# Kernel optimization log

Hardware: AMD Instinct MI355X
Metric: run time of the kernel (lower is better)

## Reference

```python
import jax, jax.numpy as jnp
import numpy as np

DIM = 768
HEADS = 12
HD = DIM // HEADS
E = 8
R = 64
ALPHA = 128.0
LORA_SCALE = ALPHA / R  # 2.0
ENABLE_BITS = np.array([1.0, 0.0, 1.0], dtype=np.float32)  # LoRA on q and v slices of qkv


def setup_inputs() -> dict:
    key = jax.random.key(0)
    ks = jax.random.split(key, 8)
    x = jax.random.normal(ks[0], (2, 4096, DIM), jnp.float32)
    # base (frozen) weights, shared across experts; no biases (qkv_bias=False)
    Wqkv = jax.random.normal(ks[1], (3 * DIM, DIM), jnp.float32) * 0.02
    Wproj = jax.random.normal(ks[2], (DIM, DIM), jnp.float32) * 0.02
    # per-expert LoRA adapters. qkv: shared down-proj A, per-output-slice up-proj B,
    # masked by enable bits (q,k,v).
    Aqkv = jax.random.normal(ks[3], (E, R, DIM), jnp.float32) * 0.02
    Bqkv = jax.random.normal(ks[4], (E, 3, DIM, R), jnp.float32) * 0.02
    Bqkv = Bqkv * jnp.asarray(ENABLE_BITS)[None, :, None, None]
    Aproj = jax.random.normal(ks[5], (E, R, DIM), jnp.float32) * 0.02
    Bproj = jax.random.normal(ks[6], (E, DIM, R), jnp.float32) * 0.02
    expert_indices = np.arange(4, dtype=np.int64) % E  # static per-chunk routing
    chunk_sizes = np.array([1024, 1024, 1024, 1024], dtype=np.int64)
    return {"x": x, "Wqkv": Wqkv, "Aqkv": Aqkv, "Bqkv": Bqkv, "Wproj": Wproj,
            "Aproj": Aproj, "Bproj": Bproj, "expert_indices": expert_indices,
            "chunk_sizes": chunk_sizes}


def reference(x, Wqkv, Aqkv, Bqkv, Wproj, Aproj, Bproj, expert_indices, chunk_sizes):
    # chunk sizes / expert indices are static host-side routing metadata
    sizes = [int(c) for c in np.asarray(chunk_sizes)]
    eidx = [int(e) for e in np.asarray(expert_indices)]
    offs = np.concatenate([[0], np.cumsum(sizes)])
    B = x.shape[0]
    scale = HD ** -0.5
    last_k = None
    last_v = None
    outs = []
    for i, n in enumerate(sizes):
        xc = x[:, offs[i]:offs[i + 1]]            # [B, n, DIM]
        e = eidx[i]
        # LoRA-adapted qkv for this chunk's expert
        base = xc @ Wqkv.T                        # [B, n, 3*DIM]
        h = xc @ Aqkv[e].T                        # [B, n, R]
        delta = jnp.einsum('bnr,tdr->bntd', h, Bqkv[e]).reshape(B, n, 3 * DIM)
        qkv = (base + LORA_SCALE * delta).reshape(B, n, 3, HEADS, HD)
        qkv = qkv.transpose(2, 0, 3, 1, 4)        # [3, B, H, n, HD]
        q, k, v = qkv[0], qkv[1], qkv[2]
        if last_k is not None:                    # growing KV over chunks (chunk-causal)
            k = jnp.concatenate([last_k, k], axis=-2)
            v = jnp.concatenate([last_v, v], axis=-2)
        last_k, last_v = k, v
        attn = jax.nn.softmax(jnp.einsum('bhqd,bhkd->bhqk', q * scale, k), axis=-1)
        o = jnp.einsum('bhqk,bhkd->bhqd', attn, v)
        o = o.transpose(0, 2, 1, 3).reshape(B, n, DIM)
        # LoRA-adapted output projection for the same expert
        o = o @ Wproj.T + LORA_SCALE * ((o @ Aproj[e].T) @ Bproj[e].T)
        outs.append(o)
    return jnp.concatenate(outs, axis=1)          # [B, total, DIM]
```

## Files before the change

### kernel.cpp

```cpp
#include <hip/hip_runtime.h>
#include <math.h>

#define BATCH   2
#define SEQ     4096
#define DIMD    768
#define NHEADS  12
#define HDIM    64
#define RR      64
#define CHUNK   1024
#define NTOK    (BATCH * SEQ)
#define BHN     (BATCH * NHEADS)
#define KC2     2304
#define QSCALE  0.18033688011112042f

typedef __attribute__((ext_vector_type(8))) short short8;
typedef __attribute__((ext_vector_type(4))) float f32x4;

#define AS1 __attribute__((address_space(1)))
#define AS3 __attribute__((address_space(3)))

__device__ __forceinline__ void glds16(const void* g, void* l) {
    __builtin_amdgcn_global_load_lds((const AS1 unsigned int*)g,
                                     (AS3 unsigned int*)l, 16, 0, 0);
}

__device__ __forceinline__ unsigned short f2bf(float x) {
    union { float f; unsigned u; } c; c.f = x;
    unsigned u = c.u + 0x7fffu + ((c.u >> 16) & 1u);
    return (unsigned short)(u >> 16);
}
__device__ __forceinline__ float bf2f(unsigned short h) {
    union { unsigned u; float f; } c; c.u = ((unsigned)h) << 16;
    return c.f;
}
__device__ __forceinline__ unsigned pack2bf(float a, float b) {
    union { float f; unsigned u; } x, y; x.f = a; y.f = b;
    unsigned ua = x.u + 0x7fffu + ((x.u >> 16) & 1u);
    unsigned ub = y.u + 0x7fffu + ((y.u >> 16) & 1u);
    return (ua >> 16) | (ub & 0xffff0000u);
}

__global__ __launch_bounds__(256)
void combine_split(const float* __restrict__ W, const float* __restrict__ A,
                   const float* __restrict__ Bm, int NB,
                   unsigned short* __restrict__ out)
{
    const int tid = threadIdx.x;
    const int ty = tid >> 4, tx = tid & 15;
    const int f0 = blockIdx.x * 64, d0 = blockIdx.y * 64, e = blockIdx.z;

    __shared__ float Bb[64][68];
    __shared__ float Aa[64][68];

    const float* Ae = A + (long)e * RR * DIMD;
    const float* Be = Bm + (long)e * NB * RR;

    const int lrow = tid >> 2, lc = (tid & 3) * 16;
    #pragma unroll
    for (int u = 0; u < 16; u += 4) {
        *(float4*)&Bb[lrow][lc + u] = *(const float4*)&Be[(long)(f0 + lrow) * RR + lc + u];
        *(float4*)&Aa[lrow][lc + u] = *(const float4*)&Ae[(long)lrow * DIMD + d0 + lc + u];
    }
    __syncthreads();

    float acc[4][4] = {};
    #pragma unroll 4
    for (int r = 0; r < RR; r++) {
        const float4 bv = *(float4*)&Aa[r][tx * 4];
        #pragma unroll
        for (int i = 0; i < 4; i++) {
            const float av = Bb[ty + 16 * i][r];
            acc[i][0] = fmaf(av, bv.x, acc[i][0]);
            acc[i][1] = fmaf(av, bv.y, acc[i][1]);
            acc[i][2] = fmaf(av, bv.z, acc[i][2]);
            acc[i][3] = fmaf(av, bv.w, acc[i][3]);
        }
    }

    #pragma unroll
    for (int i = 0; i < 4; i++) {
        const int f = f0 + ty + 16 * i;
        const int d = d0 + tx * 4;
        unsigned short* o = out + ((long)e * NB + f) * KC2 + d;
        const float4 wv = *(const float4*)&W[(long)f * DIMD + d];
        const float v0 = wv.x + 2.0f * acc[i][0];
        const float v1 = wv.y + 2.0f * acc[i][1];
        const float v2 = wv.z + 2.0f * acc[i][2];
        const float v3 = wv.w + 2.0f * acc[i][3];
        const unsigned short h0 = f2bf(v0), h1 = f2bf(v1);
        const unsigned short h2 = f2bf(v2), h3 = f2bf(v3);
        uint2 hp, lp;
        hp.x = (unsigned)h0 | ((unsigned)h1 << 16);
        hp.y = (unsigned)h2 | ((unsigned)h3 << 16);
        lp.x = pack2bf(v0 - bf2f(h0), v1 - bf2f(h1));
        lp.y = pack2bf(v2 - bf2f(h2), v3 - bf2f(h3));
        *(uint2*)&o[0]    = hp;
        *(uint2*)&o[768]  = lp;
        *(uint2*)&o[1536] = hp;
    }
}

__global__ __launch_bounds__(192)
void build_xa2(const float* __restrict__ X, unsigned short* __restrict__ out)
{
    const int tok = blockIdx.x;
    const int j = threadIdx.x * 4;
    const float* xr = X + (long)tok * DIMD;
    unsigned short* o = out + (long)tok * KC2;
    float4 v = *(const float4*)&xr[j];
    unsigned short h0 = f2bf(v.x), h1 = f2bf(v.y), h2 = f2bf(v.z), h3 = f2bf(v.w);
    uint2 hp, lp;
    hp.x = (unsigned)h0 | ((unsigned)h1 << 16);
    hp.y = (unsigned)h2 | ((unsigned)h3 << 16);
    lp.x = pack2bf(v.x - bf2f(h0), v.y - bf2f(h1));
    lp.y = pack2bf(v.z - bf2f(h2), v.w - bf2f(h3));
    *(uint2*)&o[j] = hp;
    *(uint2*)&o[768 + j] = hp;
    *(uint2*)&o[1536 + j] = lp;
}

template<int MODE>
__global__ __launch_bounds__(256)
void mfma_gemm(const unsigned short* __restrict__ A,
               const unsigned short* __restrict__ B, int NB, int n_base,
               unsigned short* __restrict__ qpl, unsigned short* __restrict__ kpl,
               unsigned short* __restrict__ vpl, float* __restrict__ outf)
{
    __shared__ __align__(16) unsigned short lA[128 * 64];
    __shared__ __align__(16) unsigned short lB[128 * 64];

    const int tid = threadIdx.x;
    const int lane = tid & 63;
    const int wave = tid >> 6;
    const int n = lane & 15;
    const int quad = lane >> 4;
    const int wm = wave & 1, wn = wave >> 1;

    const int m0 = blockIdx.x * 128;
    const int n0 = n_base + blockIdx.y * 128;
    const int e = (m0 & (SEQ - 1)) >> 10;
    const unsigned short* Ap = A + (long)m0 * KC2;
    const unsigned short* Bp = B + ((long)e * NB + n0) * KC2;

    long soff[4];
    int sldsoff = wave * 1024;
    #pragma unroll
    for (int iss = 0; iss < 4; iss++) {
        const int g = iss * 256 + tid;
        const int row = g >> 3;
        const int gc = (g & 7) ^ (row & 7);
        soff[iss] = (long)row * KC2 + gc * 8;
    }

    f32x4 acc[4][4];
    #pragma unroll
    for (int i = 0; i < 4; i++)
        #pragma unroll
        for (int j = 0; j < 4; j++)
            acc[i][j] = (f32x4){0.f, 0.f, 0.f, 0.f};

    for (int k0 = 0; k0 < KC2; k0 += 64) {
        __syncthreads();
        #pragma unroll
        for (int iss = 0; iss < 4; iss++) {
            glds16(Ap + soff[iss] + k0, (char*)lA + iss * 4096 + sldsoff);
            glds16(Bp + soff[iss] + k0, (char*)lB + iss * 4096 + sldsoff);
        }
        __builtin_amdgcn_s_waitcnt(0);
        __syncthreads();

        #pragma unroll
        for (int kk = 0; kk < 2; kk++) {
            const int kg = kk * 4;
            short8 af[4], bfr[4];
            #pragma unroll
            for (int mt = 0; mt < 4; mt++) {
                const int r = wm * 64 + mt * 16 + n;
                const int p = (kg + quad) ^ (r & 7);
                af[mt] = *(const short8*)&lA[r * 64 + p * 8];
            }
            #pragma unroll
            for (int nt = 0; nt < 4; nt++) {
                const int r = wn * 64 + nt * 16 + n;
                const int p = (kg + quad) ^ (r & 7);
                bfr[nt] = *(const short8*)&lB[r * 64 + p * 8];
            }
            #pragma unroll
            for (int mt = 0; mt < 4; mt++)
                #pragma unroll
                for (int nt = 0; nt < 4; nt++) {
                    if (MODE == 1)
                        acc[mt][nt] = __builtin_amdgcn_mfma_f32_16x16x32_bf16(
                            af[mt], bfr[nt], acc[mt][nt], 0, 0, 0);
                    else
                        acc[mt][nt] = __builtin_amdgcn_mfma_f32_16x16x32_bf16(
                            bfr[nt], af[mt], acc[mt][nt], 0, 0, 0);
                }
        }
    }

    #pragma unroll
    for (int mt = 0; mt < 4; mt++) {
        #pragma unroll
        for (int nt = 0; nt < 4; nt++) {
            f32x4 a = acc[mt][nt];
            if (MODE == 0) {
                const int fb = n0 + wn * 64 + nt * 16 + quad * 4;
                const int t = fb >= 768 ? 1 : 0;
                const int rem = fb - t * 768;
                const int head = rem >> 6;
                const int d0 = rem & 63;
                const int token = m0 + wm * 64 + mt * 16 + n;
                const int b = token >> 12, s = token & (SEQ - 1);
                const int bh = b * NHEADS + head;
                const float sc = t ? 1.0f : QSCALE;
                unsigned short* dst = (t ? kpl : qpl) + ((long)(bh * SEQ + s)) * HDIM + d0;
                uint2 pk;
                pk.x = pack2bf(a[0] * sc, a[1] * sc);
                pk.y = pack2bf(a[2] * sc, a[3] * sc);
                *(uint2*)dst = pk;
            } else if (MODE == 1) {
                const int f = n0 + wn * 64 + nt * 16 + n;
                const int head = (f - 1536) >> 6;
                const int d = f & 63;
                const int tok0 = m0 + wm * 64 + mt * 16 + quad * 4;
                const int b = tok0 >> 12, s0 = tok0 & (SEQ - 1);
                const int bh = b * NHEADS + head;
                unsigned short* dst = vpl + ((long)(bh * HDIM + d)) * SEQ + s0;
                uint2 pk;
                pk.x = pack2bf(a[0], a[1]);
                pk.y = pack2bf(a[2], a[3]);
                *(uint2*)dst = pk;
            } else {
                const int fb = n0 + wn * 64 + nt * 16 + quad * 4;
                const int token = m0 + wm * 64 + mt * 16 + n;
                *(f32x4*)&outf[(long)token * DIMD + fb] = a;
            }
        }
    }
}

__global__ __launch_bounds__(256)
void attn_split(const unsigned short* __restrict__ qp,
                const unsigned short* __restrict__ kpl,
                const unsigned short* __restrict__ vtp,
                unsigned short* __restrict__ XA,
                float* __restrict__ pO, float* __restrict__ pl)
{
    __shared__ __align__(16) unsigned short lK[64 * 64];
    __shared__ __align__(16) unsigned short lV[64 * 64];
    __shared__ __align__(16) unsigned short lP[4][32 * 64];

    const int tid = threadIdx.x;
    const int lane = tid & 63;
    const int wave = tid >> 6;
    const int n = lane & 15;
    const int quad = lane >> 4;
    const int c7 = n & 7;

    const int qb = blockIdx.x;
    const int bh = blockIdx.y;
    const int z = blockIdx.z;
    int ci, ks0, klen, pidx;
    switch (z) {
        case 0:  ci = 3; ks0 = 0;    klen = 2048; pidx = 0;  break;
        case 1:  ci = 3; ks0 = 2048; klen = 2048; pidx = 1;  break;
        case 2:  ci = 2; ks0 = 0;    klen = 2048; pidx = 2;  break;
        case 3:  ci = 1; ks0 = 0;    klen = 2048; pidx = -1; break;
        case 4:  ci = 2; ks0 = 2048; klen = 1024; pidx = 3;  break;
        default: ci = 0; ks0 = 0;    klen = 1024; pidx = -1; break;
    }
    const int b = bh / NHEADS;
    const int h = bh - b * NHEADS;

    const long planeQK = (long)bh * SEQ * HDIM;
    const long planeVt = (long)bh * HDIM * SEQ;
    const int qch = qb * 128 + wave * 32;
    const int q0 = ci * CHUNK + qch;

    long skoff[2], svoff[2];
    #pragma unroll
    for (int p = 0; p < 2; p++) {
        const int g = (wave * 2 + p) * 64 + lane;
        const int row = g >> 3;
        const int gc = (g & 7) ^ (row & 7);
        skoff[p] = (long)row * HDIM + gc * 8;
        svoff[p] = (long)row * SEQ + gc * 8;
    }

    short8 qf[2][2];
    #pragma unroll
    for (int qt = 0; qt < 2; qt++)
        #pragma unroll
        for (int s = 0; s < 2; s++)
            qf[qt][s] = *(const short8*)&qp[planeQK + (long)(q0 + qt * 16 + n) * HDIM + s * 32 + quad * 8];

    const short8 ones8 = {0x3f80, 0x3f80, 0x3f80, 0x3f80, 0x3f80, 0x3f80, 0x3f80, 0x3f80};

    f32x4 acc[4][2];
    f32x4 accl[2];
    #pragma unroll
    for (int m2 = 0; m2 < 4; m2++) {
        acc[m2][0] = (f32x4){0.f, 0.f, 0.f, 0.f};
        acc[m2][1] = (f32x4){0.f, 0.f, 0.f, 0.f};
    }
    accl[0] = (f32x4){0.f, 0.f, 0.f, 0.f};
    accl[1] = (f32x4){0.f, 0.f, 0.f, 0.f};

    unsigned short* Pw = &lP[wave][0];

    for (int k0 = ks0; k0 < ks0 + klen; k0 += 64) {
        __syncthreads();
        glds16(kpl + planeQK + (long)k0 * HDIM + skoff[0], (char*)lK + wave * 2048);
        glds16(kpl + planeQK + (long)k0 * HDIM + skoff[1], (char*)lK + wave * 2048 + 1024);
        glds16(vtp + planeVt + k0 + svoff[0], (char*)lV + wave * 2048);
        glds16(vtp + planeVt + k0 + svoff[1], (char*)lV + wave * 2048 + 1024);
        __builtin_amdgcn_s_waitcnt(0);
        __syncthreads();

        f32x4 st[4][2];
        #pragma unroll
        for (int kt = 0; kt < 4; kt++) {
            st[kt][0] = (f32x4){0.f, 0.f, 0.f, 0.f};
            st[kt][1] = (f32x4){0.f, 0.f, 0.f, 0.f};
        }
        #pragma unroll
        for (int s = 0; s < 2; s++) {
            #pragma unroll
            for (int kt = 0; kt < 4; kt++) {
                const int gr = (s * 4 + quad) ^ c7;
                short8 kf = *(const short8*)&lK[(kt * 16 + n) * 64 + gr * 8];
                st[kt][0] = __builtin_amdgcn_mfma_f32_16x16x32_bf16(kf, qf[0][s], st[kt][0], 0, 0, 0);
                st[kt][1] = __builtin_amdgcn_mfma_f32_16x16x32_bf16(kf, qf[1][s], st[kt][1], 0, 0, 0);
            }
        }

        #pragma unroll
        for (int qt = 0; qt < 2; qt++) {
            unsigned short* prow = Pw + (qt * 16 + n) * 64;
            #pragma unroll
            for (int kt = 0; kt < 4; kt++) {
                const unsigned u0 = __float_as_uint(__builtin_exp2f(st[kt][qt][0])) + 0x8000u;
                const unsigned u1 = __float_as_uint(__builtin_exp2f(st[kt][qt][1])) + 0x8000u;
                const unsigned u2 = __float_as_uint(__builtin_exp2f(st[kt][qt][2])) + 0x8000u;
                const unsigned u3 = __float_as_uint(__builtin_exp2f(st[kt][qt][3])) + 0x8000u;
                uint2 pkv;
                pkv.x = __builtin_amdgcn_perm(u1, u0, 0x07060302);
                pkv.y = __builtin_amdgcn_perm(u3, u2, 0x07060302);
                const int gsw = (2 * kt + (quad >> 1)) ^ c7;
                *(uint2*)&prow[gsw * 8 + (quad & 1) * 4] = pkv;
            }
        }

        #pragma unroll
        for (int hh = 0; hh < 2; hh++) {
            short8 pf[2];
            #pragma unroll
            for (int qt = 0; qt < 2; qt++) {
                const int gsw = (hh * 4 + quad) ^ c7;
                pf[qt] = *(const short8*)&Pw[(qt * 16 + n) * 64 + gsw * 8];
            }
            #pragma unroll
            for (int m2 = 0; m2 < 4; m2++) {
                const int gr = (hh * 4 + quad) ^ c7;
                short8 vf = *(const short8*)&lV[(m2 * 16 + n) * 64 + gr * 8];
                acc[m2][0] = __builtin_amdgcn_mfma_f32_16x16x32_bf16(vf, pf[0], acc[m2][0], 0, 0, 0);
                acc[m2][1] = __builtin_amdgcn_mfma_f32_16x16x32_bf16(vf, pf[1], acc[m2][1], 0, 0, 0);
            }
            accl[0] = __builtin_amdgcn_mfma_f32_16x16x32_bf16(ones8, pf[0], accl[0], 0, 0, 0);
            accl[1] = __builtin_amdgcn_mfma_f32_16x16x32_bf16(ones8, pf[1], accl[1], 0, 0, 0);
        }
    }

    if (pidx < 0) {
        #pragma unroll
        for (int qt = 0; qt < 2; qt++) {
            const float inv = 1.0f / accl[qt][0];
            const int token = b * SEQ + q0 + qt * 16 + n;
            unsigned short* xrow = XA + (long)token * KC2;
            #pragma unroll
            for (int m2 = 0; m2 < 4; m2++) {
                const int d = h * HDIM + m2 * 16 + quad * 4;
                const float o0 = acc[m2][qt][0] * inv;
                const float o1 = acc[m2][qt][1] * inv;
                const float o2 = acc[m2][qt][2] * inv;
                const float o3 = acc[m2][qt][3] * inv;
                const unsigned short h0 = f2bf(o0), h1 = f2bf(o1);
                const unsigned short h2 = f2bf(o2), h3 = f2bf(o3);
                uint2 hp, lp;
                hp.x = (unsigned)h0 | ((unsigned)h1 << 16);
                hp.y = (unsigned)h2 | ((unsigned)h3 << 16);
                lp.x = pack2bf(o0 - bf2f(h0), o1 - bf2f(h1));
                lp.y = pack2bf(o2 - bf2f(h2), o3 - bf2f(h3));
                *(uint2*)&xrow[d] = hp;
                *(uint2*)&xrow[768 + d] = hp;
                *(uint2*)&xrow[1536 + d] = lp;
            }
        }
    } else {
        const long pq = (long)(pidx * BHN + bh) * 1024 + qch;
        #pragma unroll
        for (int qt = 0; qt < 2; qt++) {
            const long qoff = (pq + qt * 16 + n) * 64;
            #pragma unroll
            for (int m2 = 0; m2 < 4; m2++)
                *(f32x4*)&pO[qoff + m2 * 16 + quad * 4] = acc[m2][qt];
            if (quad == 0)
                pl[pq + qt * 16 + n] = accl[qt][0];
        }
    }
}

__global__ __launch_bounds__(256)
void attn_combine(const float* __restrict__ pO, const float* __restrict__ pl,
                  unsigned short* __restrict__ XA)
{
    const int t = threadIdx.x;
    const int g = blockIdx.x;
    const int ci = 2 + (g >> 3);
    const int qb = g & 7;
    const int bh = blockIdx.y;
    const int b = bh / NHEADS, h = bh - b * NHEADS;
    const int pA = (ci == 2) ? 2 : 0;
    const int pB = (ci == 2) ? 3 : 1;

    const int qrow = t >> 1;
    const int dh = (t & 1) * 32;
    const int qc = qb * 128 + qrow;
    const long iA = (long)(pA * BHN + bh) * 1024 + qc;
    const long iB = (long)(pB * BHN + bh) * 1024 + qc;
    const float inv = 1.0f / (pl[iA] + pl[iB]);
    const int token = b * SEQ + ci * CHUNK + qc;
    unsigned short* xrow = XA + (long)token * KC2 + h * HDIM + dh;

    #pragma unroll
    for (int u = 0; u < 8; u++) {
        const float4 a = *(const float4*)&pO[iA * 64 + dh + u * 4];
        const float4 c = *(const float4*)&pO[iB * 64 + dh + u * 4];
        const float o0 = (a.x + c.x) * inv;
        const float o1 = (a.y + c.y) * inv;
        const float o2 = (a.z + c.z) * inv;
        const float o3 = (a.w + c.w) * inv;
        const unsigned short h0 = f2bf(o0), h1 = f2bf(o1);
        const unsigned short h2 = f2bf(o2), h3 = f2bf(o3);
        uint2 hp, lp;
        hp.x = (unsigned)h0 | ((unsigned)h1 << 16);
        hp.y = (unsigned)h2 | ((unsigned)h3 << 16);
        lp.x = pack2bf(o0 - bf2f(h0), o1 - bf2f(h1));
        lp.y = pack2bf(o2 - bf2f(h2), o3 - bf2f(h3));
        *(uint2*)&xrow[u * 4] = hp;
        *(uint2*)&xrow[768 + u * 4] = hp;
        *(uint2*)&xrow[1536 + u * 4] = lp;
    }
}

extern "C" void kernel_launch(void* const* d_in, const int* in_sizes, int n_in,
                              void* d_out, int out_size, void* d_ws, size_t ws_size,
                              hipStream_t stream) {
    (void)in_sizes; (void)n_in; (void)out_size; (void)ws_size;
    const float* x     = (const float*)d_in[0];
    const float* Wqkv  = (const float*)d_in[1];
    const float* Aqkv  = (const float*)d_in[2];
    const float* Bqkv  = (const float*)d_in[3];
    const float* Wproj = (const float*)d_in[4];
    const float* Aproj = (const float*)d_in[5];
    const float* Bproj = (const float*)d_in[6];

    char* wsb = (char*)d_ws;
    unsigned short* XA   = (unsigned short*)(wsb);
    unsigned short* WBq  = (unsigned short*)(wsb + (38l << 20));
    float*          pO   = (float*)(wsb + (38l << 20));
    float*          pl   = (float*)(wsb + (63l << 20));
    unsigned short* WBp  = (unsigned short*)(wsb + (80l << 20));
    unsigned short* qpl  = (unsigned short*)(wsb + (94l << 20));
    unsigned short* kpl  = (unsigned short*)(wsb + (107l << 20));
    unsigned short* vpl  = (unsigned short*)(wsb + (120l << 20));

    dim3 blk(256);

    combine_split<<<dim3(36, 12, 4), blk, 0, stream>>>(Wqkv, Aqkv, Bqkv, 3 * DIMD, WBq);
    combine_split<<<dim3(12, 12, 4), blk, 0, stream>>>(Wproj, Aproj, Bproj, DIMD, WBp);
    build_xa2<<<dim3(NTOK), dim3(192), 0, stream>>>(x, XA);
    mfma_gemm<0><<<dim3(NTOK / 128, 12), blk, 0, stream>>>(XA, WBq, 3 * DIMD, 0,    qpl, kpl, vpl, nullptr);
    mfma_gemm<1><<<dim3(NTOK / 128, 6),  blk, 0, stream>>>(XA, WBq, 3 * DIMD, 1536, qpl, kpl, vpl, nullptr);
    attn_split<<<dim3(8, BHN, 6), blk, 0, stream>>>(qpl, kpl, vpl, XA, pO, pl);
    attn_combine<<<dim3(16, BHN), blk, 0, stream>>>(pO, pl, XA);
    mfma_gemm<2><<<dim3(NTOK / 128, 6), blk, 0, stream>>>(XA, WBp, DIMD, 0, nullptr, nullptr, nullptr, (float*)d_out);
}
```

Baseline: 412.3 us.

## Remap GEMM and attention blocks per XCD and double attention block size

The GEMM launches become 1D grids whose block IDs are remapped so that all blocks on one XCD work on the same expert and the same group of N tiles, keeping the shared B weights and A rows in that XCD's L2. The attention kernel moves to 512 threads (8 waves, 256 query rows per block), so each K/V tile loaded into LDS feeds twice as many queries, and its block IDs are likewise grouped by XCD so that each XCD handles three (batch, head) planes. The costs are more LDS per block for the P buffers, possibly lower occupancy, and a dependence on the hardware dispatching blocks round-robin across the eight XCDs.

Result: no change. 418.8 us (+1.6%).

```diff
diff --git a/kernel.cpp b/kernel.cpp
--- a/kernel.cpp
+++ b/kernel.cpp
@@ -119,7 +119,7 @@
     *(uint2*)&o[1536 + j] = lp;
 }
 
-template<int MODE>
+template<int MODE, int NBT>
 __global__ __launch_bounds__(256)
 void mfma_gemm(const unsigned short* __restrict__ A,
                const unsigned short* __restrict__ B, int NB, int n_base,
@@ -136,9 +136,16 @@
     const int quad = lane >> 4;
     const int wm = wave & 1, wn = wave >> 1;
 
-    const int m0 = blockIdx.x * 128;
-    const int n0 = n_base + blockIdx.y * 128;
-    const int e = (m0 & (SEQ - 1)) >> 10;
+    const int id = blockIdx.x;
+    const int xcd = id & 7;
+    const int loc = id >> 3;
+    const int p = xcd * (NBT / 2) + (loc >> 4);
+    const int ml = loc & 15;
+    const int e = p / NBT;
+    const int nb = p - e * NBT;
+    const int mb = ((ml >> 3) << 5) + e * 8 + (ml & 7);
+    const int m0 = mb * 128;
+    const int n0 = n_base + nb * 128;
     const unsigned short* Ap = A + (long)m0 * KC2;
     const unsigned short* Bp = B + ((long)e * NB + n0) * KC2;
 
@@ -176,14 +183,14 @@
             #pragma unroll
             for (int mt = 0; mt < 4; mt++) {
                 const int r = wm * 64 + mt * 16 + n;
-                const int p = (kg + quad) ^ (r & 7);
-                af[mt] = *(const short8*)&lA[r * 64 + p * 8];
+                const int p2 = (kg + quad) ^ (r & 7);
+                af[mt] = *(const short8*)&lA[r * 64 + p2 * 8];
             }
             #pragma unroll
             for (int nt = 0; nt < 4; nt++) {
                 const int r = wn * 64 + nt * 16 + n;
-                const int p = (kg + quad) ^ (r & 7);
-                bfr[nt] = *(const short8*)&lB[r * 64 + p * 8];
+                const int p2 = (kg + quad) ^ (r & 7);
+                bfr[nt] = *(const short8*)&lB[r * 64 + p2 * 8];
             }
             #pragma unroll
             for (int mt = 0; mt < 4; mt++)
@@ -240,7 +247,7 @@
     }
 }
 
-__global__ __launch_bounds__(256)
+__global__ __launch_bounds__(512)
 void attn_split(const unsigned short* __restrict__ qp,
                 const unsigned short* __restrict__ kpl,
                 const unsigned short* __restrict__ vtp,
@@ -249,7 +256,7 @@
 {
     __shared__ __align__(16) unsigned short lK[64 * 64];
     __shared__ __align__(16) unsigned short lV[64 * 64];
-    __shared__ __align__(16) unsigned short lP[4][32 * 64];
+    __shared__ __align__(16) unsigned short lP[8][32 * 64];
 
     const int tid = threadIdx.x;
     const int lane = tid & 63;
@@ -258,9 +265,15 @@
     const int quad = lane >> 4;
     const int c7 = n & 7;
 
-    const int qb = blockIdx.x;
-    const int bh = blockIdx.y;
-    const int z = blockIdx.z;
+    const int id = blockIdx.x;
+    const int xcd = id & 7;
+    const int loc = id >> 3;
+    const int sub = loc % 3;
+    const int r2 = loc / 3;
+    const int z = r2 % 6;
+    const int qb = r2 / 6;
+    const int bh = xcd * 3 + sub;
+
     int ci, ks0, klen, pidx;
     switch (z) {
         case 0:  ci = 3; ks0 = 0;    klen = 2048; pidx = 0;  break;
@@ -275,17 +288,15 @@
 
     const long planeQK = (long)bh * SEQ * HDIM;
     const long planeVt = (long)bh * HDIM * SEQ;
-    const int qch = qb * 128 + wave * 32;
+    const int qch = qb * 256 + wave * 32;
     const int q0 = ci * CHUNK + qch;
 
-    long skoff[2], svoff[2];
-    #pragma unroll
-    for (int p = 0; p < 2; p++) {
-        const int g = (wave * 2 + p) * 64 + lane;
-        const int row = g >> 3;
-        const int gc = (g & 7) ^ (row & 7);
-        skoff[p] = (long)row * HDIM + gc * 8;
-        svoff[p] = (long)row * SEQ + gc * 8;
+    long skoff, svoff;
+    {
+        const int row = tid >> 3;
+        const int gc = (tid & 7) ^ (row & 7);
+        skoff = (long)row * HDIM + gc * 8;
+        svoff = (long)row * SEQ + gc * 8;
     }
 
     short8 qf[2][2];
@@ -311,10 +322,8 @@
 
     for (int k0 = ks0; k0 < ks0 + klen; k0 += 64) {
         __syncthreads();
-        glds16(kpl + planeQK + (long)k0 * HDIM + skoff[0], (char*)lK + wave * 2048);
-        glds16(kpl + planeQK + (long)k0 * HDIM + skoff[1], (char*)lK + wave * 2048 + 1024);
-        glds16(vtp + planeVt + k0 + svoff[0], (char*)lV + wave * 2048);
-        glds16(vtp + planeVt + k0 + svoff[1], (char*)lV + wave * 2048 + 1024);
+        glds16(kpl + planeQK + (long)k0 * HDIM + skoff, (char*)lK + wave * 1024);
+        glds16(vtp + planeVt + k0 + svoff, (char*)lV + wave * 1024);
         __builtin_amdgcn_s_waitcnt(0);
         __syncthreads();
 
@@ -481,9 +490,9 @@
     combine_split<<<dim3(36, 12, 4), blk, 0, stream>>>(Wqkv, Aqkv, Bqkv, 3 * DIMD, WBq);
     combine_split<<<dim3(12, 12, 4), blk, 0, stream>>>(Wproj, Aproj, Bproj, DIMD, WBp);
     build_xa2<<<dim3(NTOK), dim3(192), 0, stream>>>(x, XA);
-    mfma_gemm<0><<<dim3(NTOK / 128, 12), blk, 0, stream>>>(XA, WBq, 3 * DIMD, 0,    qpl, kpl, vpl, nullptr);
-    mfma_gemm<1><<<dim3(NTOK / 128, 6),  blk, 0, stream>>>(XA, WBq, 3 * DIMD, 1536, qpl, kpl, vpl, nullptr);
-    attn_split<<<dim3(8, BHN, 6), blk, 0, stream>>>(qpl, kpl, vpl, XA, pO, pl);
+    mfma_gemm<0, 12><<<dim3(768), blk, 0, stream>>>(XA, WBq, 3 * DIMD, 0,    qpl, kpl, vpl, nullptr);
+    mfma_gemm<1, 6><<<dim3(384),  blk, 0, stream>>>(XA, WBq, 3 * DIMD, 1536, qpl, kpl, vpl, nullptr);
+    attn_split<<<dim3(576), dim3(512), 0, stream>>>(qpl, kpl, vpl, XA, pO, pl);
     attn_combine<<<dim3(16, BHN), blk, 0, stream>>>(pO, pl, XA);
-    mfma_gemm<2><<<dim3(NTOK / 128, 6), blk, 0, stream>>>(XA, WBp, DIMD, 0, nullptr, nullptr, nullptr, (float*)d_out);
-}
+    mfma_gemm<2, 6><<<dim3(384), blk, 0, stream>>>(XA, WBp, DIMD, 0, nullptr, nullptr, nullptr, (float*)d_out);
+}
```
